# Kernel tuning notes

Measured on AMD Instinct MI355X. Metric: run time of the kernel, lower is better.

## Reference

```python
import jax, jax.numpy as jnp
import numpy as np

N = 8192
IN_F = 512
OUT_F = 256

def setup_inputs() -> dict:
    key = jax.random.key(0)
    k1, k2, k3 = jax.random.split(key, 3)
    A = jax.random.uniform(k1, (N, N), dtype=jnp.float32)
    X = jax.random.normal(k2, (N, IN_F), dtype=jnp.float32)
    init_range = np.sqrt(6.0 / (IN_F + OUT_F)).astype(np.float32)
    W = jax.random.uniform(k3, (IN_F, OUT_F), dtype=jnp.float32,
                           minval=-init_range, maxval=init_range)
    return {"weighted_adjacency_matrix": A, "feature_matrix": X, "weight": W}

def reference(weighted_adjacency_matrix, feature_matrix, weight):
    A = weighted_adjacency_matrix
    # d = (1 + row_sum(A))^{-1/2}; D^{-1/2} A D^{-1/2} via row/col broadcast scaling
    d = jax.lax.rsqrt(1.0 + jnp.sum(A, axis=1))            # [N]
    norm_adj = d[:, None] * A * d[None, :]                  # [N, N]
    support = feature_matrix @ weight                       # [N, out_features]
    return norm_adj @ support                               # [N, out_features]
```

## Files before the change

kernel.cpp:

```cpp
#include <hip/hip_runtime.h>
#include <hip/hip_bf16.h>
#include <stdint.h>

#define NROW 8192
#define INF  512
#define OUTF 256

typedef __attribute__((ext_vector_type(8))) short bf16x8;
typedef __attribute__((ext_vector_type(4))) float f32x4;

__device__ __forceinline__ unsigned short f2bf(float x) {
  union { float f; unsigned u; } v; v.f = x;
  unsigned r = v.u + 0x7fffu + ((v.u >> 16) & 1u);
  return (unsigned short)(r >> 16);
}
__device__ __forceinline__ unsigned short f2bf_fast(float x) {
  union { float f; unsigned u; } v; v.f = x;
  return (unsigned short)((v.u + 0x8000u) >> 16);
}
__device__ __forceinline__ float bf2f(unsigned short h) {
  union { unsigned u; float f; } v; v.u = ((unsigned)h) << 16;
  return v.f;
}

__device__ __forceinline__ void async_cp16(const void* g, void* l) {
  __builtin_amdgcn_global_load_lds((const __attribute__((address_space(1))) void*)g,
                                   (__attribute__((address_space(3))) void*)l,
                                   16, 0, 0);
}

__global__ __launch_bounds__(256) void k_rowsum_cvt(
    const float* __restrict__ A, float* __restrict__ dv,
    unsigned short* __restrict__ Abf) {
  int w = threadIdx.x >> 6, lane = threadIdx.x & 63;
  int row = blockIdx.x * 4 + w;
  const f32x4* ar = (const f32x4*)(A + (size_t)row * NROW);
  ushort4* br = (ushort4*)(Abf + (size_t)row * NROW);
  float s = 0.f;
  #pragma unroll 4
  for (int it = 0; it < NROW / 256; ++it) {
    f32x4 v = __builtin_nontemporal_load(&ar[it * 64 + lane]);
    s += (v.x + v.y) + (v.z + v.w);
    ushort4 b;
    b.x = f2bf(v.x); b.y = f2bf(v.y); b.z = f2bf(v.z); b.w = f2bf(v.w);
    br[it * 64 + lane] = b;
  }
  #pragma unroll
  for (int off = 32; off > 0; off >>= 1) s += __shfl_down(s, off, 64);
  if (lane == 0) dv[row] = rsqrtf(1.f + s);
}

__global__ __launch_bounds__(256) void k_rowsum(
    const float* __restrict__ A, float* __restrict__ dv) {
  int w = threadIdx.x >> 6, lane = threadIdx.x & 63;
  int row = blockIdx.x * 4 + w;
  const f32x4* ar = (const f32x4*)(A + (size_t)row * NROW);
  float s = 0.f;
  #pragma unroll 4
  for (int it = 0; it < NROW / 256; ++it) {
    f32x4 v = __builtin_nontemporal_load(&ar[it * 64 + lane]);
    s += (v.x + v.y) + (v.z + v.w);
  }
  #pragma unroll
  for (int off = 32; off > 0; off >>= 1) s += __shfl_down(s, off, 64);
  if (lane == 0) dv[row] = rsqrtf(1.f + s);
}

__global__ __launch_bounds__(256) void k_convert_w(
    const float* __restrict__ W, unsigned short* __restrict__ WsT) {
  int idx = blockIdx.x * 256 + threadIdx.x;
  int k = idx >> 8, f = idx & 255;
  WsT[(size_t)f * INF + k] = f2bf(W[idx]);
}

__global__ __launch_bounds__(256, 2) void k_support_fx(
    const unsigned short* __restrict__ WsT,
    const float* __restrict__ X,
    const float* __restrict__ dv,
    unsigned short* __restrict__ YT) {
  __shared__ unsigned short lA[128 * 64];
  __shared__ unsigned short lB[128 * 64];
  const int t = threadIdx.x;
  const int w = t >> 6, lane = t & 63;
  const int m0 = blockIdx.x * 128;
  const int n0 = blockIdx.y * 128;
  const int rsub = lane >> 3, csub = lane & 7, swz = csub ^ rsub;
  const int lr = lane & 15, lq = lane >> 4, x7 = lane & 7;
  const int mw = (w >> 1) * 64, nw = (w & 1) * 64;

  const int xrow = t >> 1, xhalf = t & 1;
  const float4* xsrc = (const float4*)(X + (size_t)(n0 + xrow) * INF + xhalf * 32);

  f32x4 acc[4][4];
  #pragma unroll
  for (int i = 0; i < 4; ++i)
    #pragma unroll
    for (int j = 0; j < 4; ++j) acc[i][j] = f32x4{0.f, 0.f, 0.f, 0.f};

  const unsigned short* ga0 = WsT + (size_t)(m0 + w * 8 + rsub) * INF + swz * 8;

  for (int it = 0; it < INF / 64; ++it) {
    __syncthreads();
    #pragma unroll
    for (int i = 0; i < 4; ++i)
      async_cp16(ga0 + (size_t)(i * 32) * INF + it * 64, &lA[(i * 32 + w * 8) * 64]);
    #pragma unroll
    for (int u = 0; u < 8; ++u) {
      float4 v = xsrc[it * 16 + u];
      ushort4 b;
      b.x = f2bf(v.x); b.y = f2bf(v.y); b.z = f2bf(v.z); b.w = f2bf(v.w);
      int k = xhalf * 32 + u * 4;
      int chunk = k >> 3, klo = k & 7;
      int slot = chunk ^ (xrow & 7);
      *(ushort4*)&lB[xrow * 64 + (slot << 3) + klo] = b;
    }
    __syncthreads();
    #pragma unroll
    for (int ks = 0; ks < 2; ++ks) {
      bf16x8 af[4], bfv[4];
      #pragma unroll
      for (int mi = 0; mi < 4; ++mi)
        af[mi] = *(const bf16x8*)&lA[(mw + mi * 16 + lr) * 64 + (((ks * 4 + lq) ^ x7) << 3)];
      #pragma unroll
      for (int ni = 0; ni < 4; ++ni)
        bfv[ni] = *(const bf16x8*)&lB[(nw + ni * 16 + lr) * 64 + (((ks * 4 + lq) ^ x7) << 3)];
      #pragma unroll
      for (int mi = 0; mi < 4; ++mi)
        #pragma unroll
        for (int ni = 0; ni < 4; ++ni)
          acc[mi][ni] = __builtin_amdgcn_mfma_f32_16x16x32_bf16(
              af[mi], bfv[ni], acc[mi][ni], 0, 0, 0);
    }
  }
  #pragma unroll
  for (int mi = 0; mi < 4; ++mi) {
    #pragma unroll
    for (int ni = 0; ni < 4; ++ni) {
      f32x4 a = acc[mi][ni];
      int gr0 = m0 + mw + mi * 16 + lq * 4;
      int gc  = n0 + nw + ni * 16 + lr;
      float dd = dv[gc];
      #pragma unroll
      for (int r = 0; r < 4; ++r)
        YT[(size_t)(gr0 + r) * NROW + gc] = f2bf(dd * a[r]);
    }
  }
}

__global__ __launch_bounds__(256, 2) void k_gemm_main_bf16a(
    const unsigned short* __restrict__ Abf,
    const unsigned short* __restrict__ YT,
    unsigned short* __restrict__ P) {
  __shared__ unsigned short lA[128 * 64];
  __shared__ unsigned short lB[256 * 64];
  const int t = threadIdx.x;
  const int w = t >> 6, lane = t & 63;
  const int m0 = blockIdx.x * 128;
  const int kz = blockIdx.y * 1024;
  const int rsub = lane >> 3, csub = lane & 7, swz = csub ^ rsub;
  const int lr = lane & 15, lq = lane >> 4, x7 = lane & 7;
  const int mw = (w & 1) * 64;
  const int nw = (w >> 1) * 128;

  f32x4 acc[4][8];
  #pragma unroll
  for (int i = 0; i < 4; ++i)
    #pragma unroll
    for (int j = 0; j < 8; ++j) acc[i][j] = f32x4{0.f, 0.f, 0.f, 0.f};

  const unsigned short* ga0 = Abf + (size_t)(m0 + w * 8 + rsub) * NROW + kz + swz * 8;
  const unsigned short* gb0 = YT + (size_t)(w * 8 + rsub) * NROW + kz + swz * 8;

  for (int it = 0; it < 16; ++it) {
    __syncthreads();
    #pragma unroll
    for (int i = 0; i < 8; ++i)
      async_cp16(gb0 + (size_t)(i * 32) * NROW + it * 64, &lB[(i * 32 + w * 8) * 64]);
    #pragma unroll
    for (int i = 0; i < 4; ++i)
      async_cp16(ga0 + (size_t)(i * 32) * NROW + it * 64, &lA[(i * 32 + w * 8) * 64]);
    __syncthreads();
    #pragma unroll
    for (int ks = 0; ks < 2; ++ks) {
      bf16x8 af[4], bfv[8];
      #pragma unroll
      for (int mi = 0; mi < 4; ++mi)
        af[mi] = *(const bf16x8*)&lA[(mw + mi * 16 + lr) * 64 + (((ks * 4 + lq) ^ x7) << 3)];
      #pragma unroll
      for (int ni = 0; ni < 8; ++ni)
        bfv[ni] = *(const bf16x8*)&lB[(nw + ni * 16 + lr) * 64 + (((ks * 4 + lq) ^ x7) << 3)];
      #pragma unroll
      for (int mi = 0; mi < 4; ++mi)
        #pragma unroll
        for (int ni = 0; ni < 8; ++ni)
          acc[mi][ni] = __builtin_amdgcn_mfma_f32_16x16x32_bf16(
              af[mi], bfv[ni], acc[mi][ni], 0, 0, 0);
    }
  }

  unsigned short* Pz = P + (size_t)blockIdx.y * NROW * OUTF;
  #pragma unroll
  for (int mi = 0; mi < 4; ++mi) {
    #pragma unroll
    for (int ni = 0; ni < 8; ++ni) {
      f32x4 a = acc[mi][ni];
      int gr0 = m0 + mw + mi * 16 + lq * 4;
      int gc  = nw + ni * 16 + lr;
      #pragma unroll
      for (int r = 0; r < 4; ++r)
        Pz[(size_t)(gr0 + r) * OUTF + gc] = f2bf_fast(a[r]);
    }
  }
}

__global__ __launch_bounds__(256, 2) void k_gemm_main_f32a(
    const float* __restrict__ A,
    const unsigned short* __restrict__ YT,
    unsigned short* __restrict__ P) {
  __shared__ unsigned short lA[128 * 64];
  __shared__ unsigned short lB[256 * 64];
  const int t = threadIdx.x;
  const int w = t >> 6, lane = t & 63;
  const int m0 = blockIdx.x * 128;
  const int kz = blockIdx.y * 1024;
  const int rsub = lane >> 3, csub = lane & 7, swz = csub ^ rsub;
  const int lr = lane & 15, lq = lane >> 4, x7 = lane & 7;
  const int mw = (w & 1) * 64;
  const int nw = (w >> 1) * 128;

  const int arow = t >> 2, aq = t & 3;
  const int aklo = (aq & 1) * 4;

  f32x4 acc[4][8];
  #pragma unroll
  for (int i = 0; i < 4; ++i)
    #pragma unroll
    for (int j = 0; j < 8; ++j) acc[i][j] = f32x4{0.f, 0.f, 0.f, 0.f};

  const unsigned short* gb0 = YT + (size_t)(w * 8 + rsub) * NROW + kz + swz * 8;

  for (int it = 0; it < 16; ++it) {
    __syncthreads();
    #pragma unroll
    for (int i = 0; i < 8; ++i)
      async_cp16(gb0 + (size_t)(i * 32) * NROW + it * 64, &lB[(i * 32 + w * 8) * 64]);
    #pragma unroll
    for (int h = 0; h < 2; ++h) {
      int r = arow + h * 64;
      const float4* asrc = (const float4*)(A + (size_t)(m0 + r) * NROW + kz + it * 64);
      #pragma unroll
      for (int j = 0; j < 4; ++j) {
        float4 v = asrc[aq + 4 * j];
        ushort4 b;
        b.x = f2bf_fast(v.x); b.y = f2bf_fast(v.y);
        b.z = f2bf_fast(v.z); b.w = f2bf_fast(v.w);
        int chunk = (aq + 4 * j) >> 1;
        int slot = chunk ^ (r & 7);
        *(ushort4*)&lA[r * 64 + (slot << 3) + aklo] = b;
      }
    }
    __syncthreads();
    #pragma unroll
    for (int ks = 0; ks < 2; ++ks) {
      bf16x8 af[4], bfv[8];
      #pragma unroll
      for (int mi = 0; mi < 4; ++mi)
        af[mi] = *(const bf16x8*)&lA[(mw + mi * 16 + lr) * 64 + (((ks * 4 + lq) ^ x7) << 3)];
      #pragma unroll
      for (int ni = 0; ni < 8; ++ni)
        bfv[ni] = *(const bf16x8*)&lB[(nw + ni * 16 + lr) * 64 + (((ks * 4 + lq) ^ x7) << 3)];
      #pragma unroll
      for (int mi = 0; mi < 4; ++mi)
        #pragma unroll
        for (int ni = 0; ni < 8; ++ni)
          acc[mi][ni] = __builtin_amdgcn_mfma_f32_16x16x32_bf16(
              af[mi], bfv[ni], acc[mi][ni], 0, 0, 0);
    }
  }

  unsigned short* Pz = P + (size_t)blockIdx.y * NROW * OUTF;
  #pragma unroll
  for (int mi = 0; mi < 4; ++mi) {
    #pragma unroll
    for (int ni = 0; ni < 8; ++ni) {
      f32x4 a = acc[mi][ni];
      int gr0 = m0 + mw + mi * 16 + lq * 4;
      int gc  = nw + ni * 16 + lr;
      #pragma unroll
      for (int r = 0; r < 4; ++r)
        Pz[(size_t)(gr0 + r) * OUTF + gc] = f2bf_fast(a[r]);
    }
  }
}

__global__ __launch_bounds__(256) void k_reduce8(
    const ushort4* __restrict__ P4, const float* __restrict__ dv,
    float4* __restrict__ o4) {
  int q = blockIdx.x * 256 + threadIdx.x;
  const int QT = NROW * OUTF / 4;
  float4 s = {0.f, 0.f, 0.f, 0.f};
  #pragma unroll
  for (int z = 0; z < 8; ++z) {
    ushort4 v = P4[(size_t)z * QT + q];
    s.x += bf2f(v.x); s.y += bf2f(v.y); s.z += bf2f(v.z); s.w += bf2f(v.w);
  }
  float dd = dv[q >> 6];
  s.x *= dd; s.y *= dd; s.z *= dd; s.w *= dd;
  o4[q] = s;
}

__global__ __launch_bounds__(256) void k_support_naive(
    const float* __restrict__ X, const float* __restrict__ W,
    const float* __restrict__ dv, float* __restrict__ Y) {
  __shared__ float lX[INF];
  int i = blockIdx.x;
  for (int k = threadIdx.x; k < INF; k += 256) lX[k] = X[(size_t)i * INF + k];
  __syncthreads();
  int f = threadIdx.x;
  float s = 0.f;
  for (int k = 0; k < INF; ++k) s += lX[k] * W[(size_t)k * OUTF + f];
  Y[(size_t)i * OUTF + f] = dv[i] * s;
}

__global__ __launch_bounds__(256) void k_main_naive(
    const float* __restrict__ A, const float* __restrict__ Y,
    const float* __restrict__ dv, float* __restrict__ out) {
  __shared__ float lA[256];
  int i = blockIdx.x, f = threadIdx.x;
  float s = 0.f;
  for (int jb = 0; jb < NROW; jb += 256) {
    __syncthreads();
    lA[threadIdx.x] = A[(size_t)i * NROW + jb + threadIdx.x];
    __syncthreads();
    for (int jj = 0; jj < 256; ++jj) s += lA[jj] * Y[(size_t)(jb + jj) * OUTF + f];
  }
  out[(size_t)i * OUTF + f] = dv[i] * s;
}

extern "C" void kernel_launch(void* const* d_in, const int* in_sizes, int n_in,
                              void* d_out, int out_size, void* d_ws, size_t ws_size,
                              hipStream_t stream) {
  const float* A = (const float*)d_in[0];
  const float* X = (const float*)d_in[1];
  const float* W = (const float*)d_in[2];
  float* out = (float*)d_out;

  const size_t SZ_YT  = (size_t)OUTF * NROW * 2;
  const size_t SZ_WST = (size_t)OUTF * INF * 2;
  const size_t SZ_D   = (size_t)NROW * 4;
  const size_t SZ_P   = (size_t)8 * NROW * OUTF * 2;
  const size_t SZ_ABF = (size_t)NROW * NROW * 2;
  const size_t NEED_BASE = SZ_YT + SZ_WST + SZ_D + SZ_P;
  const size_t NEED_FULL = NEED_BASE + SZ_ABF;

  char* p = (char*)d_ws;
  if (ws_size >= NEED_FULL) {
    unsigned short* YT  = (unsigned short*)p; p += SZ_YT;
    unsigned short* WsT = (unsigned short*)p; p += SZ_WST;
    float* dv = (float*)p; p += SZ_D;
    unsigned short* P = (unsigned short*)p; p += SZ_P;
    unsigned short* Abf = (unsigned short*)p;

    k_convert_w<<<dim3(512), dim3(256), 0, stream>>>(W, WsT);
    k_rowsum_cvt<<<dim3(2048), dim3(256), 0, stream>>>(A, dv, Abf);
    k_support_fx<<<dim3(2, 64), dim3(256), 0, stream>>>(WsT, X, dv, YT);
    k_gemm_main_bf16a<<<dim3(64, 8), dim3(256), 0, stream>>>(Abf, YT, P);
    k_reduce8<<<dim3(2048), dim3(256), 0, stream>>>((const ushort4*)P, dv, (float4*)out);
  } else if (ws_size >= NEED_BASE) {
    unsigned short* YT  = (unsigned short*)p; p += SZ_YT;
    unsigned short* WsT = (unsigned short*)p; p += SZ_WST;
    float* dv = (float*)p; p += SZ_D;
    unsigned short* P = (unsigned short*)p;

    k_convert_w<<<dim3(512), dim3(256), 0, stream>>>(W, WsT);
    k_rowsum<<<dim3(2048), dim3(256), 0, stream>>>(A, dv);
    k_support_fx<<<dim3(2, 64), dim3(256), 0, stream>>>(WsT, X, dv, YT);
    k_gemm_main_f32a<<<dim3(64, 8), dim3(256), 0, stream>>>(A, YT, P);
    k_reduce8<<<dim3(2048), dim3(256), 0, stream>>>((const ushort4*)P, dv, (float4*)out);
  } else {
    float* dv = (float*)p; p += SZ_D;
    float* Y  = (float*)p;
    k_rowsum<<<dim3(2048), dim3(256), 0, stream>>>(A, dv);
    k_support_naive<<<dim3(8192), dim3(256), 0, stream>>>(X, W, dv, Y);
    k_main_naive<<<dim3(8192), dim3(256), 0, stream>>>(A, Y, dv, out);
  }
}
```

Baseline: 432.0 us.

## Double-buffer main GEMM LDS tiles with 8 waves and fuse W conversion

```diff
diff --git a/kernel.cpp b/kernel.cpp
--- a/kernel.cpp
+++ b/kernel.cpp
@@ -29,9 +29,15 @@
                                    16, 0, 0);
 }
 
-__global__ __launch_bounds__(256) void k_rowsum_cvt(
-    const float* __restrict__ A, float* __restrict__ dv,
-    unsigned short* __restrict__ Abf) {
+__global__ __launch_bounds__(256) void k_rowsum_cvt_w(
+    const float* __restrict__ A, const float* __restrict__ W,
+    float* __restrict__ dv, unsigned short* __restrict__ Abf,
+    unsigned short* __restrict__ WsT) {
+  if (blockIdx.x < 512) {
+    int idx = blockIdx.x * 256 + threadIdx.x;
+    int k = idx >> 8, f = idx & 255;
+    WsT[(size_t)f * INF + k] = f2bf(W[idx]);
+  }
   int w = threadIdx.x >> 6, lane = threadIdx.x & 63;
   int row = blockIdx.x * 4 + w;
   const f32x4* ar = (const f32x4*)(A + (size_t)row * NROW);
@@ -147,12 +153,47 @@
   }
 }
 
-__global__ __launch_bounds__(256, 2) void k_gemm_main_bf16a(
+
+__device__ __forceinline__ void g_stage(
+    const unsigned short* ga, const unsigned short* gb, int it,
+    unsigned short* dA, unsigned short* dB, int w) {
+  #pragma unroll
+  for (int i = 0; i < 2; ++i)
+    async_cp16(ga + (size_t)(i * 64) * NROW + it * 64, &dA[(i * 64 + w * 8) * 64]);
+  #pragma unroll
+  for (int i = 0; i < 4; ++i)
+    async_cp16(gb + (size_t)(i * 64) * NROW + it * 64, &dB[(i * 64 + w * 8) * 64]);
+}
+
+__device__ __forceinline__ void g_compute(
+    const unsigned short* sA, const unsigned short* sB,
+    f32x4 (&acc)[4][4], int mw, int nw, int lr, int lq, int x7) {
+  #pragma unroll
+  for (int ks = 0; ks < 2; ++ks) {
+    bf16x8 af[4], bfv[4];
+    #pragma unroll
+    for (int mi = 0; mi < 4; ++mi)
+      af[mi] = *(const bf16x8*)&sA[(mw + mi * 16 + lr) * 64 + (((ks * 4 + lq) ^ x7) << 3)];
+    #pragma unroll
+    for (int ni = 0; ni < 4; ++ni)
+      bfv[ni] = *(const bf16x8*)&sB[(nw + ni * 16 + lr) * 64 + (((ks * 4 + lq) ^ x7) << 3)];
+    #pragma unroll
+    for (int mi = 0; mi < 4; ++mi)
+      #pragma unroll
+      for (int ni = 0; ni < 4; ++ni)
+        acc[mi][ni] = __builtin_amdgcn_mfma_f32_16x16x32_bf16(
+            af[mi], bfv[ni], acc[mi][ni], 0, 0, 0);
+  }
+}
+
+__global__ __launch_bounds__(512, 2) void k_gemm_main_v2(
     const unsigned short* __restrict__ Abf,
     const unsigned short* __restrict__ YT,
     unsigned short* __restrict__ P) {
-  __shared__ unsigned short lA[128 * 64];
-  __shared__ unsigned short lB[256 * 64];
+  __shared__ unsigned short lA0[128 * 64];
+  __shared__ unsigned short lB0[256 * 64];
+  __shared__ unsigned short lA1[128 * 64];
+  __shared__ unsigned short lB1[256 * 64];
   const int t = threadIdx.x;
   const int w = t >> 6, lane = t & 63;
   const int m0 = blockIdx.x * 128;
@@ -160,49 +201,36 @@
   const int rsub = lane >> 3, csub = lane & 7, swz = csub ^ rsub;
   const int lr = lane & 15, lq = lane >> 4, x7 = lane & 7;
   const int mw = (w & 1) * 64;
-  const int nw = (w >> 1) * 128;
-
-  f32x4 acc[4][8];
+  const int nw = (w >> 1) * 64;
+
+  f32x4 acc[4][4];
   #pragma unroll
   for (int i = 0; i < 4; ++i)
     #pragma unroll
-    for (int j = 0; j < 8; ++j) acc[i][j] = f32x4{0.f, 0.f, 0.f, 0.f};
+    for (int j = 0; j < 4; ++j) acc[i][j] = f32x4{0.f, 0.f, 0.f, 0.f};
 
   const unsigned short* ga0 = Abf + (size_t)(m0 + w * 8 + rsub) * NROW + kz + swz * 8;
   const unsigned short* gb0 = YT + (size_t)(w * 8 + rsub) * NROW + kz + swz * 8;
 
-  for (int it = 0; it < 16; ++it) {
-    __syncthreads();
-    #pragma unroll
-    for (int i = 0; i < 8; ++i)
-      async_cp16(gb0 + (size_t)(i * 32) * NROW + it * 64, &lB[(i * 32 + w * 8) * 64]);
-    #pragma unroll
-    for (int i = 0; i < 4; ++i)
-      async_cp16(ga0 + (size_t)(i * 32) * NROW + it * 64, &lA[(i * 32 + w * 8) * 64]);
-    __syncthreads();
-    #pragma unroll
-    for (int ks = 0; ks < 2; ++ks) {
-      bf16x8 af[4], bfv[8];
-      #pragma unroll
-      for (int mi = 0; mi < 4; ++mi)
-        af[mi] = *(const bf16x8*)&lA[(mw + mi * 16 + lr) * 64 + (((ks * 4 + lq) ^ x7) << 3)];
-      #pragma unroll
-      for (int ni = 0; ni < 8; ++ni)
-        bfv[ni] = *(const bf16x8*)&lB[(nw + ni * 16 + lr) * 64 + (((ks * 4 + lq) ^ x7) << 3)];
-      #pragma unroll
-      for (int mi = 0; mi < 4; ++mi)
-        #pragma unroll
-        for (int ni = 0; ni < 8; ++ni)
-          acc[mi][ni] = __builtin_amdgcn_mfma_f32_16x16x32_bf16(
-              af[mi], bfv[ni], acc[mi][ni], 0, 0, 0);
-    }
+  g_stage(ga0, gb0, 0, lA0, lB0, w);
+  __syncthreads();
+
+  #pragma unroll 1
+  for (int t2 = 0; t2 < 8; ++t2) {
+    int it = 2 * t2;
+    g_stage(ga0, gb0, it + 1, lA1, lB1, w);
+    g_compute(lA0, lB0, acc, mw, nw, lr, lq, x7);
+    __syncthreads();
+    if (t2 < 7) g_stage(ga0, gb0, it + 2, lA0, lB0, w);
+    g_compute(lA1, lB1, acc, mw, nw, lr, lq, x7);
+    __syncthreads();
   }
 
   unsigned short* Pz = P + (size_t)blockIdx.y * NROW * OUTF;
   #pragma unroll
   for (int mi = 0; mi < 4; ++mi) {
     #pragma unroll
-    for (int ni = 0; ni < 8; ++ni) {
+    for (int ni = 0; ni < 4; ++ni) {
       f32x4 a = acc[mi][ni];
       int gr0 = m0 + mw + mi * 16 + lq * 4;
       int gc  = nw + ni * 16 + lr;
@@ -361,10 +389,9 @@
     unsigned short* P = (unsigned short*)p; p += SZ_P;
     unsigned short* Abf = (unsigned short*)p;
 
-    k_convert_w<<<dim3(512), dim3(256), 0, stream>>>(W, WsT);
-    k_rowsum_cvt<<<dim3(2048), dim3(256), 0, stream>>>(A, dv, Abf);
+    k_rowsum_cvt_w<<<dim3(2048), dim3(256), 0, stream>>>(A, W, dv, Abf, WsT);
     k_support_fx<<<dim3(2, 64), dim3(256), 0, stream>>>(WsT, X, dv, YT);
-    k_gemm_main_bf16a<<<dim3(64, 8), dim3(256), 0, stream>>>(Abf, YT, P);
+    k_gemm_main_v2<<<dim3(64, 8), dim3(512), 0, stream>>>(Abf, YT, P);
     k_reduce8<<<dim3(2048), dim3(256), 0, stream>>>((const ushort4*)P, dv, (float4*)out);
   } else if (ws_size >= NEED_BASE) {
     unsigned short* YT  = (unsigned short*)p; p += SZ_YT;
```

Result: no change. 438.3 us (+1.5%).
